# Kernel optimization log

Hardware: AMD Instinct MI355X
Metric: run time of the kernel (lower is better)

## Reference

```python
import jax, jax.numpy as jnp
import numpy as np

B, N, E, D, O = 2, 50000, 500000, 128, 128


def setup_inputs() -> dict:
    key = jax.random.key(0)
    k1, k2, k3, k4, k5 = jax.random.split(key, 5)
    x = jax.random.normal(k1, (B, N, D), dtype=jnp.float32)
    edge_index = jax.random.randint(k2, (2, E), 0, N, dtype=jnp.int32)
    edge_attr = jax.random.normal(k3, (E, D), dtype=jnp.float32)
    W_msg = jax.random.normal(k4, (3 * D, O), dtype=jnp.float32) * 0.05
    b_msg = jnp.zeros((O,), dtype=jnp.float32)
    W_upd = jax.random.normal(k5, (O, O), dtype=jnp.float32) * 0.05
    b_upd = jnp.zeros((O,), dtype=jnp.float32)
    return {"x": x, "edge_index": edge_index, "edge_attr": edge_attr,
            "W_msg": W_msg, "b_msg": b_msg, "W_upd": W_upd, "b_upd": b_upd}


def reference(x, edge_index, edge_attr, W_msg, b_msg, W_upd, b_upd):
    # x: (B, N, D); edge_index: (2, E); edge_attr: (E, D)
    src, dst = edge_index[0], edge_index[1]
    # per-edge message input: [x_src, x_dst, edge_attr] -> (B, E, 3D)
    msg_in = jnp.concatenate(
        [x[:, src], x[:, dst], jnp.broadcast_to(edge_attr[None], (x.shape[0],) + edge_attr.shape)],
        axis=-1)
    msg = msg_in @ W_msg + b_msg  # (B, E, O)
    # scatter-sum messages into destination nodes, per batch
    agg = jax.vmap(lambda m: jax.ops.segment_sum(m, dst, num_segments=N))(msg)  # (B, N, O)
    counts = jax.ops.segment_sum(jnp.ones((dst.shape[0],), dtype=x.dtype), dst, num_segments=N)
    counts = jnp.maximum(counts, 1.0)  # clamp(min=1)
    messages = agg / counts[None, :, None]
    return messages @ W_upd + b_upd  # (B, N, O)
```

## Files before the change

### kernel.cpp

```cpp
#include <hip/hip_runtime.h>

#define BN 2
#define NN 50000
#define EE 500000
#define DD 128
#define OO 128

typedef float f2v __attribute__((ext_vector_type(2)));

__global__ __launch_bounds__(128) void wfuse_k(
    const float* __restrict__ Wm, const float* __restrict__ Wu,
    const float* __restrict__ bm, float* __restrict__ Wf,
    float* __restrict__ bmu) {
    const int o = threadIdx.x;
    const int k = blockIdx.x;
    float s = 0.0f;
    if (k < 3 * DD) {
#pragma unroll 4
        for (int j = 0; j < OO; ++j) s += Wm[k * OO + j] * Wu[j * OO + o];
        Wf[k * OO + o] = s;
    } else {
#pragma unroll 4
        for (int j = 0; j < OO; ++j) s += bm[j] * Wu[j * OO + o];
        bmu[o] = s;
    }
}

__global__ __launch_bounds__(256) void hist_k(const int* __restrict__ ei,
                                              int* __restrict__ hist) {
    int gid = blockIdx.x * 256 + threadIdx.x;
    if (gid >= EE) return;
    atomicAdd(&hist[ei[EE + gid]], 1);
}

__global__ __launch_bounds__(256) void scan1_k(const int* __restrict__ hist,
                                               int* __restrict__ bsum) {
    int i = blockIdx.x * 256 + threadIdx.x;
    int v = (i < NN) ? hist[i] : 0;
#pragma unroll
    for (int off = 32; off > 0; off >>= 1) v += __shfl_down(v, off);
    __shared__ int ws[4];
    if ((threadIdx.x & 63) == 0) ws[threadIdx.x >> 6] = v;
    __syncthreads();
    if (threadIdx.x == 0) bsum[blockIdx.x] = ws[0] + ws[1] + ws[2] + ws[3];
}

__global__ __launch_bounds__(256) void scan2_k(const int* __restrict__ bsum,
                                               int* __restrict__ ebsum,
                                               int* __restrict__ offsets,
                                               int nblk) {
    __shared__ int s[256];
    const int t = threadIdx.x;
    int v = (t < nblk) ? bsum[t] : 0;
    s[t] = v;
    __syncthreads();
    for (int off = 1; off < 256; off <<= 1) {
        int u = (t >= off) ? s[t - off] : 0;
        __syncthreads();
        s[t] += u;
        __syncthreads();
    }
    ebsum[t] = s[t] - v;
    if (t == 0) offsets[NN] = EE;
}

__global__ __launch_bounds__(256) void scan3_k(const int* __restrict__ hist,
                                               const int* __restrict__ ebsum,
                                               int* __restrict__ offsets,
                                               int* __restrict__ cursor) {
    __shared__ int s[256];
    const int t = threadIdx.x;
    const int i = blockIdx.x * 256 + t;
    int v = (i < NN) ? hist[i] : 0;
    s[t] = v;
    __syncthreads();
    for (int off = 1; off < 256; off <<= 1) {
        int u = (t >= off) ? s[t - off] : 0;
        __syncthreads();
        s[t] += u;
        __syncthreads();
    }
    int ex = s[t] - v + ebsum[blockIdx.x];
    if (i < NN) { offsets[i] = ex; cursor[i] = ex; }
}

__global__ __launch_bounds__(256) void fill_k(const int* __restrict__ ei,
                                              int* __restrict__ cursor,
                                              int2* __restrict__ ep) {
    int gid = blockIdx.x * 256 + threadIdx.x;
    if (gid >= EE) return;
    int dst = ei[EE + gid];
    int pos = atomicAdd(&cursor[dst], 1);
    ep[pos] = make_int2(gid, ei[gid]);
}

__global__ __launch_bounds__(256) void agg_k(
    const float* __restrict__ x,
    const float* __restrict__ ea,
    const int* __restrict__ offsets,
    const int2* __restrict__ ep,
    float* __restrict__ S,
    float* __restrict__ T,
    float* __restrict__ cnt)
{
    const int n = (blockIdx.x * 256 + threadIdx.x) >> 6;
    if (n >= NN) return;
    const int lane = threadIdx.x & 63;

    const int beg = offsets[n];
    const int end = offsets[n + 1];

    f2v tA = {0, 0}, s0A = {0, 0}, s1A = {0, 0};

    int j = beg;
    for (; j + 3 < end; j += 4) {
        int2 p0 = ep[j], p1 = ep[j + 1], p2 = ep[j + 2], p3 = ep[j + 3];
        f2v v0 = __builtin_nontemporal_load((const f2v*)(ea + (size_t)p0.x * DD) + lane);
        f2v v1 = __builtin_nontemporal_load((const f2v*)(ea + (size_t)p1.x * DD) + lane);
        f2v v2 = __builtin_nontemporal_load((const f2v*)(ea + (size_t)p2.x * DD) + lane);
        f2v v3 = __builtin_nontemporal_load((const f2v*)(ea + (size_t)p3.x * DD) + lane);
        f2v a0 = ((const f2v*)(x + (size_t)p0.y * DD))[lane];
        f2v a1 = ((const f2v*)(x + (size_t)p1.y * DD))[lane];
        f2v a2 = ((const f2v*)(x + (size_t)p2.y * DD))[lane];
        f2v a3 = ((const f2v*)(x + (size_t)p3.y * DD))[lane];
        f2v b0 = ((const f2v*)(x + ((size_t)NN + p0.y) * DD))[lane];
        f2v b1 = ((const f2v*)(x + ((size_t)NN + p1.y) * DD))[lane];
        f2v b2 = ((const f2v*)(x + ((size_t)NN + p2.y) * DD))[lane];
        f2v b3 = ((const f2v*)(x + ((size_t)NN + p3.y) * DD))[lane];
        tA  += v0 + v1 + v2 + v3;
        s0A += a0 + a1 + a2 + a3;
        s1A += b0 + b1 + b2 + b3;
    }
    for (; j < end; ++j) {
        int2 p = ep[j];
        f2v v = __builtin_nontemporal_load((const f2v*)(ea + (size_t)p.x * DD) + lane);
        f2v a = ((const f2v*)(x + (size_t)p.y * DD))[lane];
        f2v b = ((const f2v*)(x + ((size_t)NN + p.y) * DD))[lane];
        tA += v; s0A += a; s1A += b;
    }

    ((f2v*)(T + (size_t)n * DD))[lane] = tA;
    ((f2v*)(S + (size_t)n * DD))[lane] = s0A;
    ((f2v*)(S + ((size_t)NN + n) * DD))[lane] = s1A;
    if (lane == 0) cnt[n] = (float)(end - beg);
}

__global__ __launch_bounds__(256, 4) void gemm_k(
    const float* __restrict__ S,
    const float* __restrict__ T,
    const float* __restrict__ cnt,
    const float* __restrict__ x,
    const float* __restrict__ Wf,
    const float* __restrict__ bmu,
    const float* __restrict__ bu,
    float* __restrict__ out)
{
    __shared__ float Ast[32 * 64];
    __shared__ float Ws[32 * 132];

    const int tid = threadIdx.x;
    const int R0  = blockIdx.x * 64;
    const int tr4 = (tid >> 4) * 4;
    const int c0  = (tid & 15) * 4;

    const int sr = tid >> 2;
    const int sk = (tid & 3) * 8;
    const int Rs = R0 + sr;
    const bool svalid = Rs < BN * NN;
    const int ns = svalid ? (Rs < NN ? Rs : Rs - NN) : 0;
    const int rw = (sr + ((sk & 8) ? 16 : 0)) & 63;
    const int wr = tid >> 3;
    const int wc = (tid & 7) * 16;

    float acc[4][8];
#pragma unroll
    for (int i = 0; i < 4; ++i)
#pragma unroll
        for (int j = 0; j < 8; ++j) acc[i][j] = 0.0f;

    for (int kt = 0; kt < 12; ++kt) {
        const int kg  = kt * 32;
        const int seg = kg >> 7;
        const int off = kg - seg * 128 + sk;

        float4 a0 = {0, 0, 0, 0}, a1 = {0, 0, 0, 0};
        if (svalid) {
            if (seg == 0) {
                const float4* p = (const float4*)(S + (size_t)Rs * DD + off);
                a0 = p[0]; a1 = p[1];
            } else if (seg == 1) {
                const float c = cnt[ns];
                const float4* p = (const float4*)(x + (size_t)Rs * DD + off);
                a0 = p[0]; a1 = p[1];
                a0.x *= c; a0.y *= c; a0.z *= c; a0.w *= c;
                a1.x *= c; a1.y *= c; a1.z *= c; a1.w *= c;
            } else {
                const float4* p = (const float4*)(T + (size_t)ns * DD + off);
                a0 = p[0]; a1 = p[1];
            }
        }
        {
            const float av[8] = {a0.x, a0.y, a0.z, a0.w, a1.x, a1.y, a1.z, a1.w};
#pragma unroll
            for (int i = 0; i < 8; ++i)
                Ast[(sk + i) * 64 + rw] = av[i];
        }
        {
            const float4* wsrc = (const float4*)(Wf + (size_t)(kg + wr) * OO + wc);
            float4* wdst = (float4*)&Ws[wr * 132 + wc];
            wdst[0] = wsrc[0]; wdst[1] = wsrc[1];
            wdst[2] = wsrc[2]; wdst[3] = wsrc[3];
        }
        __syncthreads();

#pragma unroll 8
        for (int k = 0; k < 32; ++k) {
            const int ar = (tr4 + ((k & 8) ? 16 : 0)) & 63;
            const float4 a  = *(const float4*)&Ast[k * 64 + ar];
            const float4 w0 = *(const float4*)&Ws[k * 132 + c0];
            const float4 w1 = *(const float4*)&Ws[k * 132 + c0 + 64];
            const float av[4] = {a.x, a.y, a.z, a.w};
            const float wv[8] = {w0.x, w0.y, w0.z, w0.w, w1.x, w1.y, w1.z, w1.w};
#pragma unroll
            for (int i = 0; i < 4; ++i)
#pragma unroll
                for (int j = 0; j < 8; ++j)
                    acc[i][j] += av[i] * wv[j];
        }
        __syncthreads();
    }

    float4 bm0 = *(const float4*)(bmu + c0);
    float4 bm1 = *(const float4*)(bmu + 64 + c0);
    float4 bu0 = *(const float4*)(bu + c0);
    float4 bu1 = *(const float4*)(bu + 64 + c0);
#pragma unroll
    for (int i = 0; i < 4; ++i) {
        const int Rr = R0 + tr4 + i;
        if (Rr < BN * NN) {
            const int nr = (Rr < NN) ? Rr : Rr - NN;
            const float c = cnt[nr];
            const float inv = 1.0f / fmaxf(c, 1.0f);
            const float g = (c > 0.0f) ? 1.0f : 0.0f;
            float4 o0, o1;
            o0.x = acc[i][0] * inv + g * bm0.x + bu0.x;
            o0.y = acc[i][1] * inv + g * bm0.y + bu0.y;
            o0.z = acc[i][2] * inv + g * bm0.z + bu0.z;
            o0.w = acc[i][3] * inv + g * bm0.w + bu0.w;
            o1.x = acc[i][4] * inv + g * bm1.x + bu1.x;
            o1.y = acc[i][5] * inv + g * bm1.y + bu1.y;
            o1.z = acc[i][6] * inv + g * bm1.z + bu1.z;
            o1.w = acc[i][7] * inv + g * bm1.w + bu1.w;
            *(float4*)(out + (size_t)Rr * OO + c0)      = o0;
            *(float4*)(out + (size_t)Rr * OO + 64 + c0) = o1;
        }
    }
}

extern "C" void kernel_launch(void* const* d_in, const int* in_sizes, int n_in,
                              void* d_out, int out_size, void* d_ws, size_t ws_size,
                              hipStream_t stream) {
    const float* x  = (const float*)d_in[0];
    const int*   ei = (const int*)d_in[1];
    const float* ea = (const float*)d_in[2];
    const float* Wm = (const float*)d_in[3];
    const float* bm = (const float*)d_in[4];
    const float* Wu = (const float*)d_in[5];
    const float* bu = (const float*)d_in[6];
    float* out = (float*)d_out;

    float* S       = (float*)d_ws;
    float* T       = S + (size_t)BN * NN * DD;
    float* cnt     = T + (size_t)NN * DD;
    float* Wf      = cnt + NN;
    float* bmu     = Wf + 3 * DD * OO;
    int*   offsets = (int*)(bmu + OO);
    int*   cursor  = offsets + 50004;
    int*   hist    = cursor + NN;
    int*   bsum    = hist + NN;
    int*   ebsum   = bsum + 256;
    int2*  ep      = (int2*)(ebsum + 256);

    const int nscan = (NN + 255) / 256;

    hipMemsetAsync(hist, 0, NN * sizeof(int), stream);

    wfuse_k<<<3 * DD + 1, 128, 0, stream>>>(Wm, Wu, bm, Wf, bmu);
    hist_k<<<(EE + 255) / 256, 256, 0, stream>>>(ei, hist);
    scan1_k<<<nscan, 256, 0, stream>>>(hist, bsum);
    scan2_k<<<1, 256, 0, stream>>>(bsum, ebsum, offsets, nscan);
    scan3_k<<<nscan, 256, 0, stream>>>(hist, ebsum, offsets, cursor);
    fill_k<<<(EE + 255) / 256, 256, 0, stream>>>(ei, cursor, ep);

    agg_k<<<(NN + 3) / 4, 256, 0, stream>>>(x, ea, offsets, ep, S, T, cnt);

    const int nblocks = (BN * NN + 63) / 64;
    gemm_k<<<nblocks, 256, 0, stream>>>(S, T, cnt, x, Wf, bmu, bu, out);
}
```

Measured before the change: 641.9 us.

## Switch final GEMM to split-bf16 MFMA with prepacked fused weights

Replaces the FP32 FMA register-tiled GEMM with bf16 MFMA 16x16x32 instructions. Each FP32 value is split into a high and a low bf16 part, and three products (hi*hi, lo*hi, hi*lo) keep near-FP32 accuracy. The fused weights are prepacked once in wfuse_k into the MFMA fragment layout and read straight from global memory, and A tiles go to XOR-swizzled LDS. The aim is to move the GEMM compute onto matrix cores, at the cost of 3x the MFMA count, conversion overhead and slightly lower precision.

Result: faster. 560.9 us (-12.6%).

```diff
diff --git a/kernel.cpp b/kernel.cpp
--- a/kernel.cpp
+++ b/kernel.cpp
@@ -7,18 +7,30 @@
 #define OO 128
 
 typedef float f2v __attribute__((ext_vector_type(2)));
+typedef __attribute__((ext_vector_type(8))) __bf16 bf16x8;
+typedef __attribute__((ext_vector_type(4))) float f32x4;
 
 __global__ __launch_bounds__(128) void wfuse_k(
     const float* __restrict__ Wm, const float* __restrict__ Wu,
-    const float* __restrict__ bm, float* __restrict__ Wf,
-    float* __restrict__ bmu) {
+    const float* __restrict__ bm, unsigned short* __restrict__ Wph,
+    unsigned short* __restrict__ Wpl, float* __restrict__ bmu) {
     const int o = threadIdx.x;
     const int k = blockIdx.x;
     float s = 0.0f;
     if (k < 3 * DD) {
 #pragma unroll 4
         for (int j = 0; j < OO; ++j) s += Wm[k * OO + j] * Wu[j * OO + o];
-        Wf[k * OO + o] = s;
+        const unsigned int u = __float_as_uint(s);
+        const unsigned short hi = (unsigned short)(u >> 16);
+        const float r = s - __uint_as_float(u & 0xffff0000u);
+        const unsigned short lo = (unsigned short)(__float_as_uint(r) >> 16);
+        const int kstep = k >> 5;
+        const int kr = k & 31;
+        const int lane = (kr >> 3) * 16 + (o & 15);
+        const int ct = o >> 4;
+        const int idx = (((kstep * 8) + ct) * 64 + lane) * 8 + (kr & 7);
+        Wph[idx] = hi;
+        Wpl[idx] = lo;
     } else {
 #pragma unroll 4
         for (int j = 0; j < OO; ++j) s += bm[j] * Wu[j * OO + o];
@@ -150,109 +162,123 @@
     const float* __restrict__ T,
     const float* __restrict__ cnt,
     const float* __restrict__ x,
-    const float* __restrict__ Wf,
+    const unsigned short* __restrict__ Wph,
+    const unsigned short* __restrict__ Wpl,
     const float* __restrict__ bmu,
     const float* __restrict__ bu,
     float* __restrict__ out)
 {
-    __shared__ float Ast[32 * 64];
-    __shared__ float Ws[32 * 132];
+    __shared__ unsigned short Ahi[64 * 128];
+    __shared__ unsigned short Alo[64 * 128];
 
     const int tid = threadIdx.x;
-    const int R0  = blockIdx.x * 64;
-    const int tr4 = (tid >> 4) * 4;
-    const int c0  = (tid & 15) * 4;
-
-    const int sr = tid >> 2;
-    const int sk = (tid & 3) * 8;
-    const int Rs = R0 + sr;
-    const bool svalid = Rs < BN * NN;
-    const int ns = svalid ? (Rs < NN ? Rs : Rs - NN) : 0;
-    const int rw = (sr + ((sk & 8) ? 16 : 0)) & 63;
-    const int wr = tid >> 3;
-    const int wc = (tid & 7) * 16;
-
-    float acc[4][8];
-#pragma unroll
-    for (int i = 0; i < 4; ++i)
-#pragma unroll
-        for (int j = 0; j < 8; ++j) acc[i][j] = 0.0f;
-
-    for (int kt = 0; kt < 12; ++kt) {
-        const int kg  = kt * 32;
-        const int seg = kg >> 7;
-        const int off = kg - seg * 128 + sk;
-
-        float4 a0 = {0, 0, 0, 0}, a1 = {0, 0, 0, 0};
-        if (svalid) {
-            if (seg == 0) {
-                const float4* p = (const float4*)(S + (size_t)Rs * DD + off);
-                a0 = p[0]; a1 = p[1];
-            } else if (seg == 1) {
-                const float c = cnt[ns];
-                const float4* p = (const float4*)(x + (size_t)Rs * DD + off);
-                a0 = p[0]; a1 = p[1];
-                a0.x *= c; a0.y *= c; a0.z *= c; a0.w *= c;
-                a1.x *= c; a1.y *= c; a1.z *= c; a1.w *= c;
-            } else {
-                const float4* p = (const float4*)(T + (size_t)ns * DD + off);
-                a0 = p[0]; a1 = p[1];
-            }
+    const int R0 = blockIdx.x * 64;
+    const int wv = tid >> 6;
+    const int l = tid & 63;
+
+    const int srow = tid >> 2;
+    const int skq = (tid & 3) * 32;
+    const int Rs = R0 + srow;
+    const bool sv = Rs < BN * NN;
+    const int ns = sv ? (Rs < NN ? Rs : Rs - NN) : 0;
+    const int swz = (srow & 7) << 4;
+    const float cs = sv ? cnt[ns] : 0.0f;
+
+    f32x4 acc[4][2];
+#pragma unroll
+    for (int i = 0; i < 4; ++i) {
+        acc[i][0] = (f32x4){0.0f, 0.0f, 0.0f, 0.0f};
+        acc[i][1] = (f32x4){0.0f, 0.0f, 0.0f, 0.0f};
+    }
+
+    for (int seg = 0; seg < 3; ++seg) {
+        const float4* p = nullptr;
+        if (sv) {
+            p = (seg == 0) ? (const float4*)(S + (size_t)Rs * DD + skq)
+              : (seg == 1) ? (const float4*)(x + (size_t)Rs * DD + skq)
+                           : (const float4*)(T + (size_t)ns * DD + skq);
         }
-        {
-            const float av[8] = {a0.x, a0.y, a0.z, a0.w, a1.x, a1.y, a1.z, a1.w};
-#pragma unroll
-            for (int i = 0; i < 8; ++i)
-                Ast[(sk + i) * 64 + rw] = av[i];
+#pragma unroll
+        for (int j = 0; j < 4; ++j) {
+            float4 u0 = {0, 0, 0, 0}, u1 = {0, 0, 0, 0};
+            if (sv) {
+                u0 = p[2 * j];
+                u1 = p[2 * j + 1];
+                if (seg == 1) {
+                    u0.x *= cs; u0.y *= cs; u0.z *= cs; u0.w *= cs;
+                    u1.x *= cs; u1.y *= cs; u1.z *= cs; u1.w *= cs;
+                }
+            }
+            const float vv[8] = {u0.x, u0.y, u0.z, u0.w, u1.x, u1.y, u1.z, u1.w};
+            unsigned int hw[4], lw[4];
+#pragma unroll
+            for (int i = 0; i < 4; ++i) {
+                const unsigned int b0 = __float_as_uint(vv[2 * i]);
+                const unsigned int b1 = __float_as_uint(vv[2 * i + 1]);
+                const float r0 = vv[2 * i]     - __uint_as_float(b0 & 0xffff0000u);
+                const float r1 = vv[2 * i + 1] - __uint_as_float(b1 & 0xffff0000u);
+                hw[i] = (b0 >> 16) | (b1 & 0xffff0000u);
+                lw[i] = (__float_as_uint(r0) >> 16) | (__float_as_uint(r1) & 0xffff0000u);
+            }
+            const int byt = srow * 256 + (((skq + j * 8) * 2) ^ swz);
+            *(int4*)((char*)Ahi + byt) = make_int4(hw[0], hw[1], hw[2], hw[3]);
+            *(int4*)((char*)Alo + byt) = make_int4(lw[0], lw[1], lw[2], lw[3]);
         }
-        {
-            const float4* wsrc = (const float4*)(Wf + (size_t)(kg + wr) * OO + wc);
-            float4* wdst = (float4*)&Ws[wr * 132 + wc];
-            wdst[0] = wsrc[0]; wdst[1] = wsrc[1];
-            wdst[2] = wsrc[2]; wdst[3] = wsrc[3];
+        __syncthreads();
+
+#pragma unroll
+        for (int ks = 0; ks < 4; ++ks) {
+            bf16x8 ah[4], al[4];
+#pragma unroll
+            for (int rt = 0; rt < 4; ++rt) {
+                const int row = rt * 16 + (l & 15);
+                const int rb = row * 256 +
+                               ((ks * 64 + (l >> 4) * 16) ^ ((row & 7) << 4));
+                ah[rt] = *(const bf16x8*)((const char*)Ahi + rb);
+                al[rt] = *(const bf16x8*)((const char*)Alo + rb);
+            }
+            const int kg = seg * 4 + ks;
+#pragma unroll
+            for (int ct = 0; ct < 2; ++ct) {
+                const size_t fi =
+                    (size_t)(((kg * 8) + (wv * 2 + ct)) * 64 + l) * 8;
+                const bf16x8 wh = *(const bf16x8*)(Wph + fi);
+                const bf16x8 wl = *(const bf16x8*)(Wpl + fi);
+#pragma unroll
+                for (int rt = 0; rt < 4; ++rt) {
+                    acc[rt][ct] = __builtin_amdgcn_mfma_f32_16x16x32_bf16(
+                        ah[rt], wh, acc[rt][ct], 0, 0, 0);
+                    acc[rt][ct] = __builtin_amdgcn_mfma_f32_16x16x32_bf16(
+                        al[rt], wh, acc[rt][ct], 0, 0, 0);
+                    acc[rt][ct] = __builtin_amdgcn_mfma_f32_16x16x32_bf16(
+                        ah[rt], wl, acc[rt][ct], 0, 0, 0);
+                }
+            }
         }
         __syncthreads();
-
-#pragma unroll 8
-        for (int k = 0; k < 32; ++k) {
-            const int ar = (tr4 + ((k & 8) ? 16 : 0)) & 63;
-            const float4 a  = *(const float4*)&Ast[k * 64 + ar];
-            const float4 w0 = *(const float4*)&Ws[k * 132 + c0];
-            const float4 w1 = *(const float4*)&Ws[k * 132 + c0 + 64];
-            const float av[4] = {a.x, a.y, a.z, a.w};
-            const float wv[8] = {w0.x, w0.y, w0.z, w0.w, w1.x, w1.y, w1.z, w1.w};
-#pragma unroll
-            for (int i = 0; i < 4; ++i)
-#pragma unroll
-                for (int j = 0; j < 8; ++j)
-                    acc[i][j] += av[i] * wv[j];
-        }
-        __syncthreads();
-    }
-
-    float4 bm0 = *(const float4*)(bmu + c0);
-    float4 bm1 = *(const float4*)(bmu + 64 + c0);
-    float4 bu0 = *(const float4*)(bu + c0);
-    float4 bu1 = *(const float4*)(bu + 64 + c0);
-#pragma unroll
-    for (int i = 0; i < 4; ++i) {
-        const int Rr = R0 + tr4 + i;
-        if (Rr < BN * NN) {
-            const int nr = (Rr < NN) ? Rr : Rr - NN;
-            const float c = cnt[nr];
-            const float inv = 1.0f / fmaxf(c, 1.0f);
-            const float g = (c > 0.0f) ? 1.0f : 0.0f;
-            float4 o0, o1;
-            o0.x = acc[i][0] * inv + g * bm0.x + bu0.x;
-            o0.y = acc[i][1] * inv + g * bm0.y + bu0.y;
-            o0.z = acc[i][2] * inv + g * bm0.z + bu0.z;
-            o0.w = acc[i][3] * inv + g * bm0.w + bu0.w;
-            o1.x = acc[i][4] * inv + g * bm1.x + bu1.x;
-            o1.y = acc[i][5] * inv + g * bm1.y + bu1.y;
-            o1.z = acc[i][6] * inv + g * bm1.z + bu1.z;
-            o1.w = acc[i][7] * inv + g * bm1.w + bu1.w;
-            *(float4*)(out + (size_t)Rr * OO + c0)      = o0;
-            *(float4*)(out + (size_t)Rr * OO + 64 + c0) = o1;
+    }
+
+    const int col0 = wv * 32 + (l & 15);
+    const float bm0 = bmu[col0], bm1 = bmu[col0 + 16];
+    const float bu0 = bu[col0], bu1 = bu[col0 + 16];
+    const int rbase = (l >> 4) * 4;
+#pragma unroll
+    for (int rt = 0; rt < 4; ++rt) {
+#pragma unroll
+        for (int r = 0; r < 4; ++r) {
+            const int Rr = R0 + rt * 16 + rbase + r;
+            if (Rr < BN * NN) {
+                const int nr = (Rr < NN) ? Rr : Rr - NN;
+                const float c = cnt[nr];
+                const float inv = 1.0f / fmaxf(c, 1.0f);
+                const float g = (c > 0.0f) ? 1.0f : 0.0f;
+                __builtin_nontemporal_store(
+                    acc[rt][0][r] * inv + g * bm0 + bu0,
+                    out + (size_t)Rr * OO + col0);
+                __builtin_nontemporal_store(
+                    acc[rt][1][r] * inv + g * bm1 + bu1,
+                    out + (size_t)Rr * OO + col0 + 16);
+            }
         }
     }
 }
@@ -269,23 +295,24 @@
     const float* bu = (const float*)d_in[6];
     float* out = (float*)d_out;
 
-    float* S       = (float*)d_ws;
-    float* T       = S + (size_t)BN * NN * DD;
-    float* cnt     = T + (size_t)NN * DD;
-    float* Wf      = cnt + NN;
-    float* bmu     = Wf + 3 * DD * OO;
-    int*   offsets = (int*)(bmu + OO);
-    int*   cursor  = offsets + 50004;
-    int*   hist    = cursor + NN;
-    int*   bsum    = hist + NN;
-    int*   ebsum   = bsum + 256;
-    int2*  ep      = (int2*)(ebsum + 256);
+    float* S   = (float*)d_ws;
+    float* T   = S + (size_t)BN * NN * DD;
+    float* cnt = T + (size_t)NN * DD;
+    float* bmu = cnt + NN;
+    unsigned short* Wph = (unsigned short*)(bmu + OO);
+    unsigned short* Wpl = Wph + 3 * DD * OO;
+    int* offsets = (int*)(Wpl + 3 * DD * OO);
+    int* cursor  = offsets + 50004;
+    int* hist    = cursor + NN;
+    int* bsum    = hist + NN;
+    int* ebsum   = bsum + 256;
+    int2* ep     = (int2*)(ebsum + 256);
 
     const int nscan = (NN + 255) / 256;
 
     hipMemsetAsync(hist, 0, NN * sizeof(int), stream);
 
-    wfuse_k<<<3 * DD + 1, 128, 0, stream>>>(Wm, Wu, bm, Wf, bmu);
+    wfuse_k<<<3 * DD + 1, 128, 0, stream>>>(Wm, Wu, bm, Wph, Wpl, bmu);
     hist_k<<<(EE + 255) / 256, 256, 0, stream>>>(ei, hist);
     scan1_k<<<nscan, 256, 0, stream>>>(hist, bsum);
     scan2_k<<<1, 256, 0, stream>>>(bsum, ebsum, offsets, nscan);
@@ -295,5 +322,5 @@
     agg_k<<<(NN + 3) / 4, 256, 0, stream>>>(x, ea, offsets, ep, S, T, cnt);
 
     const int nblocks = (BN * NN + 63) / 64;
-    gemm_k<<<nblocks, 256, 0, stream>>>(S, T, cnt, x, Wf, bmu, bu, out);
-}
+    gemm_k<<<nblocks, 256, 0, stream>>>(S, T, cnt, x, Wph, Wpl, bmu, bu, out);
+}
```
